# Kernel optimization log

Hardware: AMD Instinct MI355X
Metric: run time of the kernel (lower is better)

Reference implementation:

```python
import jax, jax.numpy as jnp
import numpy as np

N_HOST, N_FLOW, E = 20000, 200000, 600000
D_IN, D_H, D_OUT = 64, 128, 32
NEG_SLOPE = 0.01  # F.leaky_relu default


def setup_inputs() -> dict:
    key = jax.random.key(0)
    ks = jax.random.split(key, 20)

    def w(k, shape):
        # kaiming-uniform-ish init scale (matches Linear fan-in scaling)
        lim = 1.0 / np.sqrt(shape[0])
        return jax.random.uniform(k, shape, jnp.float32, -lim, lim)

    return {
        "x_host": jax.random.normal(ks[0], (N_HOST, D_IN), jnp.float32),
        "x_flow": jax.random.normal(ks[1], (N_FLOW, D_IN), jnp.float32),
        "src_hf": jax.random.randint(ks[2], (E,), 0, N_HOST, dtype=jnp.int32),
        "dst_hf": jax.random.randint(ks[3], (E,), 0, N_FLOW, dtype=jnp.int32),
        "src_fh": jax.random.randint(ks[4], (E,), 0, N_FLOW, dtype=jnp.int32),
        "dst_fh": jax.random.randint(ks[5], (E,), 0, N_HOST, dtype=jnp.int32),
        "W0_hf_l": w(ks[6], (D_IN, D_H)), "W0_hf_r": w(ks[7], (D_IN, D_H)),
        "b0_hf": jnp.zeros((D_H,), jnp.float32),
        "W0_fh_l": w(ks[8], (D_IN, D_H)), "W0_fh_r": w(ks[9], (D_IN, D_H)),
        "b0_fh": jnp.zeros((D_H,), jnp.float32),
        "W1_hf_l": w(ks[10], (D_H, D_H)), "W1_hf_r": w(ks[11], (D_H, D_H)),
        "b1_hf": jnp.zeros((D_H,), jnp.float32),
        "W1_fh_l": w(ks[12], (D_H, D_H)), "W1_fh_r": w(ks[13], (D_H, D_H)),
        "b1_fh": jnp.zeros((D_H,), jnp.float32),
        "W_out": w(ks[14], (D_H, D_OUT)),
        "b_out": jnp.zeros((D_OUT,), jnp.float32),
    }


def _seg_mean(x, src, dst, n_dst):
    """Mean-aggregate src-node features over edges into n_dst segments."""
    s = jax.ops.segment_sum(x[src], dst, num_segments=n_dst)      # [n_dst, d]
    cnt = jax.ops.segment_sum(jnp.ones(src.shape, x.dtype), dst, num_segments=n_dst)
    return s / jnp.clip(cnt, 1.0)[:, None]


def _sage(x_src, x_dst, src, dst, Wl, Wr, b, n_dst):
    # SAGEConv: lin_l(mean_agg) + bias + lin_r(x_dst)
    agg = _seg_mean(x_src, src, dst, n_dst)
    return agg @ Wl + b + x_dst @ Wr


def reference(x_host, x_flow, src_hf, dst_hf, src_fh, dst_fh,
              W0_hf_l, W0_hf_r, b0_hf, W0_fh_l, W0_fh_r, b0_fh,
              W1_hf_l, W1_hf_r, b1_hf, W1_fh_l, W1_fh_r, b1_fh,
              W_out, b_out):
    lrelu = lambda v: jnp.where(v > 0, v, NEG_SLOPE * v)

    # layer 0
    h_flow = lrelu(_sage(x_host, x_flow, src_hf, dst_hf, W0_hf_l, W0_hf_r, b0_hf, N_FLOW))
    h_host = lrelu(_sage(x_flow, x_host, src_fh, dst_fh, W0_fh_l, W0_fh_r, b0_fh, N_HOST))

    # layer 1
    g_flow = lrelu(_sage(h_host, h_flow, src_hf, dst_hf, W1_hf_l, W1_hf_r, b1_hf, N_FLOW))
    g_host = lrelu(_sage(h_flow, h_host, src_fh, dst_fh, W1_fh_l, W1_fh_r, b1_fh, N_HOST))
    del g_host  # computed (matches module) but only 'flow' feeds the head

    return g_flow @ W_out + b_out  # [N_FLOW, D_OUT]
```

## Files before the change

### kernel.cpp

```cpp
#include <hip/hip_runtime.h>


#define N_HOST 20000
#define N_FLOW 200000
#define NEDGE  600000
#define D_IN   64
#define D_H    128
#define D_OUT  32
#define NSEG   (N_FLOW + N_HOST)
#define NBKT_F 196
#define NBKT_H 79
#define NBKT   (NBKT_F + NBKT_H)
#define NEB    586

typedef unsigned short u16;
typedef unsigned int   u32;
typedef short bf16x8 __attribute__((ext_vector_type(8)));
typedef float f32x4  __attribute__((ext_vector_type(4)));

__device__ __forceinline__ float bfh(u16 h) { return __uint_as_float(((u32)h) << 16); }
__device__ __forceinline__ u16 fbh(float f) {
    u32 u = __float_as_uint(f);
    return (u16)((u + 0x7fffu + ((u >> 16) & 1u)) >> 16);
}
__device__ __forceinline__ u32 packbf(float x, float y) {
    return (u32)fbh(x) | ((u32)fbh(y) << 16);
}
__device__ __forceinline__ void acc8(float* a, uint4 u) {
    a[0] += __uint_as_float(u.x << 16);
    a[1] += __uint_as_float(u.x & 0xffff0000u);
    a[2] += __uint_as_float(u.y << 16);
    a[3] += __uint_as_float(u.y & 0xffff0000u);
    a[4] += __uint_as_float(u.z << 16);
    a[5] += __uint_as_float(u.z & 0xffff0000u);
    a[6] += __uint_as_float(u.w << 16);
    a[7] += __uint_as_float(u.w & 0xffff0000u);
}

template <int U>
__device__ __forceinline__ uint4 gmean(const u16* __restrict__ pool, int rs, int coff,
                                       const int* __restrict__ gcsr,
                                       const int* __restrict__ lcsr, int st0, bool fit,
                                       int st, int en) {
    float a[8] = {0.f, 0.f, 0.f, 0.f, 0.f, 0.f, 0.f, 0.f};
    for (int e = st; e < en; e += U) {
        int n[U];
#pragma unroll
        for (int j = 0; j < U; j++)
            n[j] = (e + j < en) ? (fit ? lcsr[e + j - st0] : gcsr[e + j]) : -1;
        uint4 u[U];
#pragma unroll
        for (int j = 0; j < U; j++)
            u[j] = (n[j] >= 0) ? *(const uint4*)(pool + n[j] * rs + coff)
                               : make_uint4(0u, 0u, 0u, 0u);
#pragma unroll
        for (int j = 0; j < U; j++) acc8(a, u[j]);
    }
    float inv = (en > st) ? 1.f / (float)(en - st) : 0.f;
    uint4 o;
    o.x = packbf(a[0] * inv, a[1] * inv);
    o.y = packbf(a[2] * inv, a[3] * inv);
    o.z = packbf(a[4] * inv, a[5] * inv);
    o.w = packbf(a[6] * inv, a[7] * inv);
    return o;
}

__global__ void k_pre(const float* __restrict__ W0_hf_l, const float* __restrict__ W0_hf_r,
                      const float* __restrict__ W0_fh_l, const float* __restrict__ W0_fh_r,
                      const float* __restrict__ W1_l, const float* __restrict__ W1_r,
                      const float* __restrict__ Wout,
                      u16* __restrict__ WT0_hf, u16* __restrict__ WT0_fh,
                      u16* __restrict__ WT1_l, u16* __restrict__ WT1_r,
                      u16* __restrict__ WTo,
                      const float* __restrict__ xf, const float* __restrict__ xh,
                      u16* __restrict__ xfb, u16* __restrict__ xhb,
                      const int* __restrict__ dst_hf, const int* __restrict__ dst_fh,
                      int* __restrict__ bcnt) {
    int b = blockIdx.x, t = threadIdx.x;
    if (b < 34) {
        u16 tmp[8];
        if (b < 32) {
            int e = (b & 7) * 2048 + t * 8;
            int n = e >> 7, k0 = e & 127;
            if (b < 8) {
#pragma unroll
                for (int j = 0; j < 8; j++) {
                    int k = k0 + j;
                    tmp[j] = fbh(k < 64 ? W0_hf_l[k * D_H + n] : W0_hf_r[(k - 64) * D_H + n]);
                }
                *(uint4*)(WT0_hf + n * 128 + k0) = *(uint4*)tmp;
            } else if (b < 16) {
#pragma unroll
                for (int j = 0; j < 8; j++) {
                    int k = k0 + j;
                    tmp[j] = fbh(k < 64 ? W0_fh_l[k * D_H + n] : W0_fh_r[(k - 64) * D_H + n]);
                }
                *(uint4*)(WT0_fh + n * 128 + k0) = *(uint4*)tmp;
            } else if (b < 24) {
#pragma unroll
                for (int j = 0; j < 8; j++) tmp[j] = fbh(W1_l[(k0 + j) * D_H + n]);
                *(uint4*)(WT1_l + n * 128 + k0) = *(uint4*)tmp;
            } else {
#pragma unroll
                for (int j = 0; j < 8; j++) tmp[j] = fbh(W1_r[(k0 + j) * D_H + n]);
                *(uint4*)(WT1_r + n * 128 + k0) = *(uint4*)tmp;
            }
        } else {
            int e = (b - 32) * 2048 + t * 8;
            int n = e >> 7, k0 = e & 127;
#pragma unroll
            for (int j = 0; j < 8; j++) tmp[j] = fbh(Wout[(k0 + j) * D_OUT + n]);
            *(uint4*)(WTo + n * 128 + k0) = *(uint4*)tmp;
        }
    } else if (b < 34 + 6875) {
        int q = (b - 34) * 256 + t;
        const int TF = (N_FLOW * D_IN) / 8;
        const int TT = TF + (N_HOST * D_IN) / 8;
        if (q >= TT) return;
        const float* src; u16* dst; int base;
        if (q < TF) { src = xf; dst = xfb; base = q * 8; }
        else        { src = xh; dst = xhb; base = (q - TF) * 8; }
        float4 f0 = *(const float4*)(src + base);
        float4 f1 = *(const float4*)(src + base + 4);
        uint4 o;
        o.x = packbf(f0.x, f0.y); o.y = packbf(f0.z, f0.w);
        o.z = packbf(f1.x, f1.y); o.w = packbf(f1.z, f1.w);
        *(uint4*)(dst + base) = o;
    } else {
        __shared__ int h[NBKT];
        for (int j = t; j < NBKT; j += 256) h[j] = 0;
        __syncthreads();
        int base = (b - 34 - 6875) * 2048;
#pragma unroll
        for (int i = 0; i < 8; i++) {
            int e = base + t + i * 256;
            if (e < 2 * NEDGE) {
                int bkt = (e < NEDGE) ? (dst_hf[e] >> 10)
                                      : (NBKT_F + (dst_fh[e - NEDGE] >> 8));
                atomicAdd(&h[bkt], 1);
            }
        }
        __syncthreads();
        for (int j = t; j < NBKT; j += 256)
            if (h[j]) atomicAdd(&bcnt[j], h[j]);
    }
}

__global__ void kb2(const int* __restrict__ src_hf, const int* __restrict__ dst_hf,
                    const int* __restrict__ src_fh, const int* __restrict__ dst_fh,
                    const int* __restrict__ bcnt, int* __restrict__ bcur,
                    int2* __restrict__ binE) {
    __shared__ int sp[512];
    __shared__ int lh[NBKT];
    __shared__ int lb[NBKT];
    int t = threadIdx.x;
    int o1 = (t < NBKT) ? bcnt[t] : 0;
    int o2 = (t + 256 < NBKT) ? bcnt[t + 256] : 0;
    sp[t] = o1; sp[t + 256] = o2;
    for (int j = t; j < NBKT; j += 256) lh[j] = 0;
    __syncthreads();
    for (int d = 1; d < 512; d <<= 1) {
        int a0 = (t >= d) ? sp[t - d] : 0;
        int a1 = sp[t + 256 - d];
        __syncthreads();
        sp[t] += a0; sp[t + 256] += a1;
        __syncthreads();
    }
    sp[t] -= o1; sp[t + 256] -= o2;
    __syncthreads();
    int base = blockIdx.x * 2048;
    int mybkt[8], myrank[8], mysrc[8], mydst[8];
#pragma unroll
    for (int i = 0; i < 8; i++) {
        int e = base + t + i * 256;
        mybkt[i] = -1;
        if (e < 2 * NEDGE) {
            int s, d;
            if (e < NEDGE) { s = src_hf[e]; d = dst_hf[e]; }
            else           { s = src_fh[e - NEDGE]; d = dst_fh[e - NEDGE] + N_FLOW; }
            int bkt = (d < N_FLOW) ? (d >> 10) : (NBKT_F + ((d - N_FLOW) >> 8));
            mybkt[i] = bkt; mysrc[i] = s; mydst[i] = d;
            myrank[i] = atomicAdd(&lh[bkt], 1);
        }
    }
    __syncthreads();
    for (int j = t; j < NBKT; j += 256)
        lb[j] = lh[j] ? atomicAdd(&bcur[j], lh[j]) : 0;
    __syncthreads();
#pragma unroll
    for (int i = 0; i < 8; i++) {
        if (mybkt[i] >= 0) {
            int pos = sp[mybkt[i]] + lb[mybkt[i]] + myrank[i];
            binE[pos] = make_int2(mysrc[i], mydst[i]);
        }
    }
}

__global__ __launch_bounds__(256) void kb3(const int2* __restrict__ binE,
                                           const int* __restrict__ bcnt,
                                           int* __restrict__ off, int* __restrict__ csr) {
    __shared__ int sp[512];
    __shared__ int deg[1024];
    __shared__ int ts[256];
    int b = blockIdx.x, t = threadIdx.x;
    sp[t] = (t < NBKT) ? bcnt[t] : 0;
    sp[t + 256] = (t + 256 < NBKT) ? bcnt[t + 256] : 0;
    __syncthreads();
    for (int d = 1; d < 512; d <<= 1) {
        int a0 = (t >= d) ? sp[t - d] : 0;
        int a1 = sp[t + 256 - d];
        __syncthreads();
        sp[t] += a0; sp[t + 256] += a1;
        __syncthreads();
    }
    int e0 = (b == 0) ? 0 : sp[b - 1];
    int e1 = sp[b];
    int nbase, ncnt;
    if (b < NBKT_F) { nbase = b << 10; ncnt = min(1024, N_FLOW - nbase); }
    else { nbase = N_FLOW + ((b - NBKT_F) << 8); ncnt = min(256, NSEG - nbase); }
    for (int i = t; i < 1024; i += 256) deg[i] = 0;
    __syncthreads();
    for (int e = e0 + t; e < e1; e += 256) {
        int2 p = binE[e];
        atomicAdd(&deg[p.y - nbase], 1);
    }
    __syncthreads();
    int loc[4]; int s = 0;
#pragma unroll
    for (int j = 0; j < 4; j++) { loc[j] = s; s += deg[t * 4 + j]; }
    ts[t] = s;
    __syncthreads();
    for (int d = 1; d < 256; d <<= 1) {
        int x = (t >= d) ? ts[t - d] : 0;
        __syncthreads();
        ts[t] += x;
        __syncthreads();
    }
    int base2 = e0 + ts[t] - s;
    int dsave[4];
#pragma unroll
    for (int j = 0; j < 4; j++) dsave[j] = deg[t * 4 + j];
    __syncthreads();
#pragma unroll
    for (int j = 0; j < 4; j++) {
        int idx = t * 4 + j;
        int st = base2 + loc[j];
        deg[idx] = st;
        if (idx < ncnt) off[nbase + idx] = st + dsave[j];
    }
    __syncthreads();
    for (int e = e0 + t; e < e1; e += 256) {
        int2 p = binE[e];
        int r = atomicAdd(&deg[p.y - nbase], 1);
        csr[r] = p.x;
    }
}

__global__ __launch_bounds__(512, 4) void k_host(
    const u16* __restrict__ xfb, const u16* __restrict__ xhb,
    const int* __restrict__ off, const int* __restrict__ csr,
    const u16* __restrict__ WT0, const float* __restrict__ b0,
    const u16* __restrict__ WT1l, u16* __restrict__ hT, int M) {
    __shared__ __align__(16) u16 sA[64 * 136];
    __shared__ int sOff[72];
    __shared__ int sCsr[2560];
    const int t = threadIdx.x;
    const int m0 = blockIdx.x * 64;
    if (t < 65) {
        int idx = N_FLOW + m0 - 1 + t;
        sOff[t] = off[min(idx, NSEG - 1)];
    }
    {
        int r = t >> 3, c = t & 7;
        int row = m0 + r;
        uint4 v = make_uint4(0u, 0u, 0u, 0u);
        if (row < M) v = *(const uint4*)(xhb + row * 64 + c * 8);
        *(uint4*)(&sA[r * 136 + 64 + c * 8]) = v;
    }
    __syncthreads();
    int st0 = sOff[0];
    int win = sOff[64] - st0;
    bool fit = (win <= 2560);
    if (fit) for (int e = t; e < win; e += 512) sCsr[e] = csr[st0 + e];
    __syncthreads();
    {
        int r = t >> 3, c = t & 7;
        int row = m0 + r;
        uint4 o = make_uint4(0u, 0u, 0u, 0u);
        if (row < M) o = gmean<8>(xfb, 64, c * 8, csr, sCsr, st0, fit, sOff[r], sOff[r + 1]);
        *(uint4*)(&sA[r * 136 + c * 8]) = o;
    }
    __syncthreads();
    const int w = t >> 6, wr = w >> 1, wc = w & 1;
    const int ln = t & 63, l15 = ln & 15, quad = ln >> 4;
    const u16* pA = sA + (wr * 16 + l15) * 136 + quad * 8;
    const u16* pB0 = WT0 + wc * 8192 + l15 * 128 + quad * 8;
    f32x4 acc[4];
#pragma unroll
    for (int tt = 0; tt < 4; tt++) acc[tt] = (f32x4){0.f, 0.f, 0.f, 0.f};
#pragma unroll
    for (int s = 0; s < 4; s++) {
        bf16x8 a = *(const bf16x8*)(pA + s * 32);
#pragma unroll
        for (int tt = 0; tt < 4; tt++) {
            bf16x8 b = *(const bf16x8*)(pB0 + tt * 2048 + s * 32);
            acc[tt] = __builtin_amdgcn_mfma_f32_16x16x32_bf16(a, b, acc[tt], 0, 0, 0);
        }
    }
    __syncthreads();
#pragma unroll
    for (int tt = 0; tt < 4; tt++) {
        int col = wc * 64 + tt * 16 + l15;
        float bv = b0[col];
#pragma unroll
        for (int i = 0; i < 4; i++) {
            int rl = wr * 16 + quad * 4 + i;
            float v = acc[tt][i] + bv;
            v = v > 0.f ? v : 0.01f * v;
            sA[rl * 136 + col] = fbh(v);
        }
    }
    __syncthreads();
    const u16* pB1 = WT1l + wc * 8192 + l15 * 128 + quad * 8;
    f32x4 accB[4];
#pragma unroll
    for (int tt = 0; tt < 4; tt++) accB[tt] = (f32x4){0.f, 0.f, 0.f, 0.f};
#pragma unroll
    for (int s = 0; s < 4; s++) {
        bf16x8 a = *(const bf16x8*)(pA + s * 32);
#pragma unroll
        for (int tt = 0; tt < 4; tt++) {
            bf16x8 b = *(const bf16x8*)(pB1 + tt * 2048 + s * 32);
            accB[tt] = __builtin_amdgcn_mfma_f32_16x16x32_bf16(a, b, accB[tt], 0, 0, 0);
        }
    }
#pragma unroll
    for (int tt = 0; tt < 4; tt++) {
        int col = wc * 64 + tt * 16 + l15;
#pragma unroll
        for (int i = 0; i < 4; i++) {
            int row = m0 + wr * 16 + quad * 4 + i;
            if (row < M) hT[row * D_H + col] = fbh(accB[tt][i]);
        }
    }
}

__global__ __launch_bounds__(512, 8) void k_mega(
    const u16* __restrict__ xfb, const u16* __restrict__ xhb,
    const int* __restrict__ off, const int* __restrict__ csr,
    const u16* __restrict__ hT,
    const u16* __restrict__ WT0, const float* __restrict__ b0,
    const u16* __restrict__ WT1r, const float* __restrict__ b1,
    const u16* __restrict__ WTo, const float* __restrict__ bout,
    float* __restrict__ OUT) {
    __shared__ __align__(16) u16 sA[64 * 136];
    __shared__ __align__(16) u16 sAg[64 * 136];
    __shared__ int sOff[72];
    __shared__ int sCsr[1024];
    const int t = threadIdx.x;
    const int m0 = blockIdx.x * 64;
    if (t < 65) {
        int idx = m0 - 1 + t;
        sOff[t] = (idx < 0) ? 0 : off[idx];
    }
    {
        int r = t >> 3, c = t & 7;
        uint4 v = *(const uint4*)(xfb + (m0 + r) * 64 + c * 8);
        *(uint4*)(&sA[r * 136 + 64 + c * 8]) = v;
    }
    __syncthreads();
    int st0 = sOff[0];
    int win = sOff[64] - st0;
    bool fit = (win <= 1024);
    if (fit) for (int e = t; e < win; e += 512) sCsr[e] = csr[st0 + e];
    __syncthreads();
    {
        int r = t >> 3, c = t & 7;
        uint4 o = gmean<4>(xhb, 64, c * 8, csr, sCsr, st0, fit, sOff[r], sOff[r + 1]);
        *(uint4*)(&sA[r * 136 + c * 8]) = o;
    }
#pragma unroll
    for (int i = 0; i < 2; i++) {
        int q = t + i * 512;
        int r = q >> 4, c = q & 15;
        uint4 o = gmean<4>(hT, 128, c * 8, csr, sCsr, st0, fit, sOff[r], sOff[r + 1]);
        *(uint4*)(&sAg[r * 136 + c * 8]) = o;
    }
    __syncthreads();
    const int w = t >> 6, wr = w >> 1, wc = w & 1;
    const int ln = t & 63, l15 = ln & 15, quad = ln >> 4;
    const u16* pA = sA + (wr * 16 + l15) * 136 + quad * 8;
    const u16* pB0 = WT0 + wc * 8192 + l15 * 128 + quad * 8;
    f32x4 acc[4];
#pragma unroll
    for (int tt = 0; tt < 4; tt++) acc[tt] = (f32x4){0.f, 0.f, 0.f, 0.f};
#pragma unroll
    for (int s = 0; s < 4; s++) {
        bf16x8 a = *(const bf16x8*)(pA + s * 32);
#pragma unroll
        for (int tt = 0; tt < 4; tt++) {
            bf16x8 b = *(const bf16x8*)(pB0 + tt * 2048 + s * 32);
            acc[tt] = __builtin_amdgcn_mfma_f32_16x16x32_bf16(a, b, acc[tt], 0, 0, 0);
        }
    }
    __syncthreads();
#pragma unroll
    for (int tt = 0; tt < 4; tt++) {
        int col = wc * 64 + tt * 16 + l15;
        float bv = b0[col];
#pragma unroll
        for (int i = 0; i < 4; i++) {
            int rl = wr * 16 + quad * 4 + i;
            float v = acc[tt][i] + bv;
            v = v > 0.f ? v : 0.01f * v;
            sA[rl * 136 + col] = fbh(v);
        }
    }
    __syncthreads();
    const u16* pB1 = WT1r + wc * 8192 + l15 * 128 + quad * 8;
    f32x4 accB[4];
#pragma unroll
    for (int tt = 0; tt < 4; tt++) accB[tt] = (f32x4){0.f, 0.f, 0.f, 0.f};
#pragma unroll
    for (int s = 0; s < 4; s++) {
        bf16x8 a = *(const bf16x8*)(pA + s * 32);
#pragma unroll
        for (int tt = 0; tt < 4; tt++) {
            bf16x8 b = *(const bf16x8*)(pB1 + tt * 2048 + s * 32);
            accB[tt] = __builtin_amdgcn_mfma_f32_16x16x32_bf16(a, b, accB[tt], 0, 0, 0);
        }
    }
#pragma unroll
    for (int tt = 0; tt < 4; tt++) {
        int col = wc * 64 + tt * 16 + l15;
        float bv = b1[col];
#pragma unroll
        for (int i = 0; i < 4; i++) {
            int rl = wr * 16 + quad * 4 + i;
            float v = accB[tt][i] + bfh(sAg[rl * 136 + col]) + bv;
            v = v > 0.f ? v : 0.01f * v;
            sAg[rl * 136 + col] = fbh(v);
        }
    }
    __syncthreads();
    const u16* pG = sAg + (wr * 16 + l15) * 136 + quad * 8;
    const u16* pBo = WTo + wc * 2048 + l15 * 128 + quad * 8;
    f32x4 acc2 = (f32x4){0.f, 0.f, 0.f, 0.f};
#pragma unroll
    for (int s = 0; s < 4; s++) {
        bf16x8 g = *(const bf16x8*)(pG + s * 32);
        bf16x8 b = *(const bf16x8*)(pBo + s * 32);
        acc2 = __builtin_amdgcn_mfma_f32_16x16x32_bf16(g, b, acc2, 0, 0, 0);
    }
    {
        int col = wc * 16 + l15;
        float bv = bout[col];
#pragma unroll
        for (int i = 0; i < 4; i++) {
            int row = m0 + wr * 16 + quad * 4 + i;
            OUT[row * D_OUT + col] = acc2[i] + bv;
        }
    }
}

extern "C" void kernel_launch(void* const* d_in, const int* in_sizes, int n_in,
                              void* d_out, int out_size, void* d_ws, size_t ws_size,
                              hipStream_t stream) {
    const float* x_host  = (const float*)d_in[0];
    const float* x_flow  = (const float*)d_in[1];
    const int* src_hf  = (const int*)d_in[2];
    const int* dst_hf  = (const int*)d_in[3];
    const int* src_fh  = (const int*)d_in[4];
    const int* dst_fh  = (const int*)d_in[5];
    const float* W0_hf_l = (const float*)d_in[6];
    const float* W0_hf_r = (const float*)d_in[7];
    const float* b0_hf   = (const float*)d_in[8];
    const float* W0_fh_l = (const float*)d_in[9];
    const float* W0_fh_r = (const float*)d_in[10];
    const float* b0_fh   = (const float*)d_in[11];
    const float* W1_hf_l = (const float*)d_in[12];
    const float* W1_hf_r = (const float*)d_in[13];
    const float* b1_hf   = (const float*)d_in[14];
    const float* W_out   = (const float*)d_in[18];
    const float* b_out   = (const float*)d_in[19];
    float* out = (float*)d_out;

    char* ws = (char*)d_ws;
    int*  off    = (int*)(ws + 0);
    int*  csr    = (int*)(ws + 880000);
    u16*  hT     = (u16*)(ws + 5680000);
    u16*  xfb    = (u16*)(ws + 10800000);
    u16*  xhb    = (u16*)(ws + 36400000);
    int2* binE   = (int2*)(ws + 38960000);
    int*  bcnt   = (int*)(ws + 48560000);
    int*  bcur   = (int*)(ws + 48561280);
    u16*  WT0_hf = (u16*)(ws + 48562560);
    u16*  WT0_fh = (u16*)(ws + 48595328);
    u16*  WT1_l  = (u16*)(ws + 48628096);
    u16*  WT1_r  = (u16*)(ws + 48660864);
    u16*  WTo    = (u16*)(ws + 48693632);

    hipMemsetAsync(bcnt, 0, 2560, stream);
    k_pre<<<34 + 6875 + NEB, 256, 0, stream>>>(
        W0_hf_l, W0_hf_r, W0_fh_l, W0_fh_r, W1_hf_l, W1_hf_r, W_out,
        WT0_hf, WT0_fh, WT1_l, WT1_r, WTo,
        x_flow, x_host, xfb, xhb, dst_hf, dst_fh, bcnt);
    kb2<<<NEB, 256, 0, stream>>>(src_hf, dst_hf, src_fh, dst_fh, bcnt, bcur, binE);
    kb3<<<NBKT, 256, 0, stream>>>(binE, bcnt, off, csr);
    k_host<<<313, 512, 0, stream>>>(xfb, xhb, off, csr, WT0_fh, b0_fh, WT1_l, hT, N_HOST);
    k_mega<<<3125, 512, 0, stream>>>(xfb, xhb, off, csr, hT, WT0_hf, b0_hf,
                                     WT1_r, b1_hf, WTo, b_out, out);
}
```

Measured before the change: 344.2 us.

## Split host gather across threads, shrink host tile, fuse flow neighbor gathers

The host kernel now handles 32 rows per block over 625 blocks. Each row's neighbor list is split across two thread halves, and their partial sums are reduced through shared memory, which gives more parallelism on the high-degree host rows (about 30 edges each). The flow mega-kernel fuses its two neighbor gathers (xhb and hT) into one loop that shares the index loads, and accumulation uses packed float2 adds. k_mega launch bounds drop from 8 to 6 waves per SIMD, allowing more registers for the wider gather at the cost of occupancy.

```diff
diff --git a/kernel.cpp b/kernel.cpp
--- a/kernel.cpp
+++ b/kernel.cpp
@@ -17,6 +17,7 @@
 typedef unsigned int   u32;
 typedef short bf16x8 __attribute__((ext_vector_type(8)));
 typedef float f32x4  __attribute__((ext_vector_type(4)));
+typedef float fx2    __attribute__((ext_vector_type(2)));
 
 __device__ __forceinline__ float bfh(u16 h) { return __uint_as_float(((u32)h) << 16); }
 __device__ __forceinline__ u16 fbh(float f) {
@@ -26,42 +27,19 @@
 __device__ __forceinline__ u32 packbf(float x, float y) {
     return (u32)fbh(x) | ((u32)fbh(y) << 16);
 }
-__device__ __forceinline__ void acc8(float* a, uint4 u) {
-    a[0] += __uint_as_float(u.x << 16);
-    a[1] += __uint_as_float(u.x & 0xffff0000u);
-    a[2] += __uint_as_float(u.y << 16);
-    a[3] += __uint_as_float(u.y & 0xffff0000u);
-    a[4] += __uint_as_float(u.z << 16);
-    a[5] += __uint_as_float(u.z & 0xffff0000u);
-    a[6] += __uint_as_float(u.w << 16);
-    a[7] += __uint_as_float(u.w & 0xffff0000u);
-}
-
-template <int U>
-__device__ __forceinline__ uint4 gmean(const u16* __restrict__ pool, int rs, int coff,
-                                       const int* __restrict__ gcsr,
-                                       const int* __restrict__ lcsr, int st0, bool fit,
-                                       int st, int en) {
-    float a[8] = {0.f, 0.f, 0.f, 0.f, 0.f, 0.f, 0.f, 0.f};
-    for (int e = st; e < en; e += U) {
-        int n[U];
-#pragma unroll
-        for (int j = 0; j < U; j++)
-            n[j] = (e + j < en) ? (fit ? lcsr[e + j - st0] : gcsr[e + j]) : -1;
-        uint4 u[U];
-#pragma unroll
-        for (int j = 0; j < U; j++)
-            u[j] = (n[j] >= 0) ? *(const uint4*)(pool + n[j] * rs + coff)
-                               : make_uint4(0u, 0u, 0u, 0u);
-#pragma unroll
-        for (int j = 0; j < U; j++) acc8(a, u[j]);
-    }
-    float inv = (en > st) ? 1.f / (float)(en - st) : 0.f;
+__device__ __forceinline__ void accp(fx2* a, uint4 u) {
+    fx2 p;
+    p.x = __uint_as_float(u.x << 16); p.y = __uint_as_float(u.x & 0xffff0000u); a[0] += p;
+    p.x = __uint_as_float(u.y << 16); p.y = __uint_as_float(u.y & 0xffff0000u); a[1] += p;
+    p.x = __uint_as_float(u.z << 16); p.y = __uint_as_float(u.z & 0xffff0000u); a[2] += p;
+    p.x = __uint_as_float(u.w << 16); p.y = __uint_as_float(u.w & 0xffff0000u); a[3] += p;
+}
+__device__ __forceinline__ uint4 packp(const fx2* a, float inv) {
     uint4 o;
-    o.x = packbf(a[0] * inv, a[1] * inv);
-    o.y = packbf(a[2] * inv, a[3] * inv);
-    o.z = packbf(a[4] * inv, a[5] * inv);
-    o.w = packbf(a[6] * inv, a[7] * inv);
+    o.x = packbf(a[0].x * inv, a[0].y * inv);
+    o.y = packbf(a[1].x * inv, a[1].y * inv);
+    o.z = packbf(a[2].x * inv, a[2].y * inv);
+    o.w = packbf(a[3].x * inv, a[3].y * inv);
     return o;
 }
 
@@ -260,57 +238,78 @@
     const u16* __restrict__ xfb, const u16* __restrict__ xhb,
     const int* __restrict__ off, const int* __restrict__ csr,
     const u16* __restrict__ WT0, const float* __restrict__ b0,
-    const u16* __restrict__ WT1l, u16* __restrict__ hT, int M) {
-    __shared__ __align__(16) u16 sA[64 * 136];
-    __shared__ int sOff[72];
-    __shared__ int sCsr[2560];
+    const u16* __restrict__ WT1l, u16* __restrict__ hT) {
+    __shared__ __align__(16) u16 sA[32 * 136];
+    __shared__ __align__(16) float sP[256 * 8];
+    __shared__ int sOff[40];
+    __shared__ int sCsr[2048];
     const int t = threadIdx.x;
-    const int m0 = blockIdx.x * 64;
-    if (t < 65) {
-        int idx = N_FLOW + m0 - 1 + t;
-        sOff[t] = off[min(idx, NSEG - 1)];
-    }
-    {
+    const int m0 = blockIdx.x * 32;
+    if (t < 33) sOff[t] = off[N_FLOW + m0 - 1 + t];
+    if (t < 256) {
         int r = t >> 3, c = t & 7;
-        int row = m0 + r;
-        uint4 v = make_uint4(0u, 0u, 0u, 0u);
-        if (row < M) v = *(const uint4*)(xhb + row * 64 + c * 8);
+        uint4 v = *(const uint4*)(xhb + (m0 + r) * 64 + c * 8);
         *(uint4*)(&sA[r * 136 + 64 + c * 8]) = v;
     }
     __syncthreads();
     int st0 = sOff[0];
-    int win = sOff[64] - st0;
-    bool fit = (win <= 2560);
+    int win = sOff[32] - st0;
+    bool fit = (win <= 2048);
     if (fit) for (int e = t; e < win; e += 512) sCsr[e] = csr[st0 + e];
     __syncthreads();
-    {
-        int r = t >> 3, c = t & 7;
-        int row = m0 + r;
-        uint4 o = make_uint4(0u, 0u, 0u, 0u);
-        if (row < M) o = gmean<8>(xfb, 64, c * 8, csr, sCsr, st0, fit, sOff[r], sOff[r + 1]);
-        *(uint4*)(&sA[r * 136 + c * 8]) = o;
-    }
-    __syncthreads();
-    const int w = t >> 6, wr = w >> 1, wc = w & 1;
+    const int r = t >> 4, s8 = (t >> 3) & 1, c = t & 7;
+    const int st = sOff[r], en = sOff[r + 1];
+    fx2 a[4] = {};
+    for (int e = st + s8; e < en; e += 16) {
+        int n[8];
+#pragma unroll
+        for (int j = 0; j < 8; j++) {
+            int ee = e + 2 * j;
+            n[j] = (ee < en) ? (fit ? sCsr[ee - st0] : csr[ee]) : -1;
+        }
+        uint4 u[8];
+#pragma unroll
+        for (int j = 0; j < 8; j++)
+            u[j] = (n[j] >= 0) ? *(const uint4*)(xfb + n[j] * 64 + c * 8)
+                               : make_uint4(0u, 0u, 0u, 0u);
+#pragma unroll
+        for (int j = 0; j < 8; j++) accp(a, u[j]);
+    }
+    if (s8) {
+        float4* p = (float4*)(&sP[(r * 8 + c) * 8]);
+        p[0] = make_float4(a[0].x, a[0].y, a[1].x, a[1].y);
+        p[1] = make_float4(a[2].x, a[2].y, a[3].x, a[3].y);
+    }
+    __syncthreads();
+    if (!s8) {
+        const float4* p = (const float4*)(&sP[(r * 8 + c) * 8]);
+        float4 v0 = p[0], v1 = p[1];
+        a[0].x += v0.x; a[0].y += v0.y; a[1].x += v0.z; a[1].y += v0.w;
+        a[2].x += v1.x; a[2].y += v1.y; a[3].x += v1.z; a[3].y += v1.w;
+        float inv = (en > st) ? 1.f / (float)(en - st) : 0.f;
+        *(uint4*)(&sA[r * 136 + c * 8]) = packp(a, inv);
+    }
+    __syncthreads();
+    const int w = t >> 6, wr = w >> 2, wc = w & 3;
     const int ln = t & 63, l15 = ln & 15, quad = ln >> 4;
     const u16* pA = sA + (wr * 16 + l15) * 136 + quad * 8;
-    const u16* pB0 = WT0 + wc * 8192 + l15 * 128 + quad * 8;
-    f32x4 acc[4];
-#pragma unroll
-    for (int tt = 0; tt < 4; tt++) acc[tt] = (f32x4){0.f, 0.f, 0.f, 0.f};
+    const u16* pB0 = WT0 + wc * 4096 + l15 * 128 + quad * 8;
+    f32x4 acc[2];
+    acc[0] = (f32x4){0.f, 0.f, 0.f, 0.f};
+    acc[1] = (f32x4){0.f, 0.f, 0.f, 0.f};
 #pragma unroll
     for (int s = 0; s < 4; s++) {
-        bf16x8 a = *(const bf16x8*)(pA + s * 32);
-#pragma unroll
-        for (int tt = 0; tt < 4; tt++) {
+        bf16x8 av = *(const bf16x8*)(pA + s * 32);
+#pragma unroll
+        for (int tt = 0; tt < 2; tt++) {
             bf16x8 b = *(const bf16x8*)(pB0 + tt * 2048 + s * 32);
-            acc[tt] = __builtin_amdgcn_mfma_f32_16x16x32_bf16(a, b, acc[tt], 0, 0, 0);
-        }
-    }
-    __syncthreads();
-#pragma unroll
-    for (int tt = 0; tt < 4; tt++) {
-        int col = wc * 64 + tt * 16 + l15;
+            acc[tt] = __builtin_amdgcn_mfma_f32_16x16x32_bf16(av, b, acc[tt], 0, 0, 0);
+        }
+    }
+    __syncthreads();
+#pragma unroll
+    for (int tt = 0; tt < 2; tt++) {
+        int col = wc * 32 + tt * 16 + l15;
         float bv = b0[col];
 #pragma unroll
         for (int i = 0; i < 4; i++) {
@@ -321,31 +320,31 @@
         }
     }
     __syncthreads();
-    const u16* pB1 = WT1l + wc * 8192 + l15 * 128 + quad * 8;
-    f32x4 accB[4];
-#pragma unroll
-    for (int tt = 0; tt < 4; tt++) accB[tt] = (f32x4){0.f, 0.f, 0.f, 0.f};
+    const u16* pB1 = WT1l + wc * 4096 + l15 * 128 + quad * 8;
+    f32x4 accB[2];
+    accB[0] = (f32x4){0.f, 0.f, 0.f, 0.f};
+    accB[1] = (f32x4){0.f, 0.f, 0.f, 0.f};
 #pragma unroll
     for (int s = 0; s < 4; s++) {
-        bf16x8 a = *(const bf16x8*)(pA + s * 32);
-#pragma unroll
-        for (int tt = 0; tt < 4; tt++) {
+        bf16x8 av = *(const bf16x8*)(pA + s * 32);
+#pragma unroll
+        for (int tt = 0; tt < 2; tt++) {
             bf16x8 b = *(const bf16x8*)(pB1 + tt * 2048 + s * 32);
-            accB[tt] = __builtin_amdgcn_mfma_f32_16x16x32_bf16(a, b, accB[tt], 0, 0, 0);
-        }
-    }
-#pragma unroll
-    for (int tt = 0; tt < 4; tt++) {
-        int col = wc * 64 + tt * 16 + l15;
+            accB[tt] = __builtin_amdgcn_mfma_f32_16x16x32_bf16(av, b, accB[tt], 0, 0, 0);
+        }
+    }
+#pragma unroll
+    for (int tt = 0; tt < 2; tt++) {
+        int col = wc * 32 + tt * 16 + l15;
 #pragma unroll
         for (int i = 0; i < 4; i++) {
             int row = m0 + wr * 16 + quad * 4 + i;
-            if (row < M) hT[row * D_H + col] = fbh(accB[tt][i]);
-        }
-    }
-}
-
-__global__ __launch_bounds__(512, 8) void k_mega(
+            hT[row * D_H + col] = fbh(accB[tt][i]);
+        }
+    }
+}
+
+__global__ __launch_bounds__(512, 6) void k_mega(
     const u16* __restrict__ xfb, const u16* __restrict__ xhb,
     const int* __restrict__ off, const int* __restrict__ csr,
     const u16* __restrict__ hT,
@@ -375,16 +374,38 @@
     if (fit) for (int e = t; e < win; e += 512) sCsr[e] = csr[st0 + e];
     __syncthreads();
     {
-        int r = t >> 3, c = t & 7;
-        uint4 o = gmean<4>(xhb, 64, c * 8, csr, sCsr, st0, fit, sOff[r], sOff[r + 1]);
-        *(uint4*)(&sA[r * 136 + c * 8]) = o;
-    }
-#pragma unroll
-    for (int i = 0; i < 2; i++) {
-        int q = t + i * 512;
-        int r = q >> 4, c = q & 15;
-        uint4 o = gmean<4>(hT, 128, c * 8, csr, sCsr, st0, fit, sOff[r], sOff[r + 1]);
-        *(uint4*)(&sAg[r * 136 + c * 8]) = o;
+        const int r = t >> 3, c = t & 7;
+        const int st = sOff[r], en = sOff[r + 1];
+        fx2 a0[4] = {}, a1[4] = {}, a2[4] = {};
+        for (int e = st; e < en; e += 4) {
+            int n[4];
+#pragma unroll
+            for (int j = 0; j < 4; j++)
+                n[j] = (e + j < en) ? (fit ? sCsr[e + j - st0] : csr[e + j]) : -1;
+            uint4 ux[4], ua[4], ub[4];
+#pragma unroll
+            for (int j = 0; j < 4; j++) {
+                if (n[j] >= 0) {
+                    const u16* px = xhb + n[j] * 64 + c * 8;
+                    const u16* ph = hT + n[j] * 128 + c * 16;
+                    ux[j] = *(const uint4*)px;
+                    ua[j] = *(const uint4*)ph;
+                    ub[j] = *(const uint4*)(ph + 8);
+                } else {
+                    ux[j] = make_uint4(0u, 0u, 0u, 0u);
+                    ua[j] = make_uint4(0u, 0u, 0u, 0u);
+                    ub[j] = make_uint4(0u, 0u, 0u, 0u);
+                }
+            }
+#pragma unroll
+            for (int j = 0; j < 4; j++) {
+                accp(a0, ux[j]); accp(a1, ua[j]); accp(a2, ub[j]);
+            }
+        }
+        float inv = (en > st) ? 1.f / (float)(en - st) : 0.f;
+        *(uint4*)(&sA[r * 136 + c * 8]) = packp(a0, inv);
+        *(uint4*)(&sAg[r * 136 + c * 16]) = packp(a1, inv);
+        *(uint4*)(&sAg[r * 136 + c * 16 + 8]) = packp(a2, inv);
     }
     __syncthreads();
     const int w = t >> 6, wr = w >> 1, wc = w & 1;
@@ -396,11 +417,11 @@
     for (int tt = 0; tt < 4; tt++) acc[tt] = (f32x4){0.f, 0.f, 0.f, 0.f};
 #pragma unroll
     for (int s = 0; s < 4; s++) {
-        bf16x8 a = *(const bf16x8*)(pA + s * 32);
+        bf16x8 av = *(const bf16x8*)(pA + s * 32);
 #pragma unroll
         for (int tt = 0; tt < 4; tt++) {
             bf16x8 b = *(const bf16x8*)(pB0 + tt * 2048 + s * 32);
-            acc[tt] = __builtin_amdgcn_mfma_f32_16x16x32_bf16(a, b, acc[tt], 0, 0, 0);
+            acc[tt] = __builtin_amdgcn_mfma_f32_16x16x32_bf16(av, b, acc[tt], 0, 0, 0);
         }
     }
     __syncthreads();
@@ -423,11 +444,11 @@
     for (int tt = 0; tt < 4; tt++) accB[tt] = (f32x4){0.f, 0.f, 0.f, 0.f};
 #pragma unroll
     for (int s = 0; s < 4; s++) {
-        bf16x8 a = *(const bf16x8*)(pA + s * 32);
+        bf16x8 av = *(const bf16x8*)(pA + s * 32);
 #pragma unroll
         for (int tt = 0; tt < 4; tt++) {
             bf16x8 b = *(const bf16x8*)(pB1 + tt * 2048 + s * 32);
-            accB[tt] = __builtin_amdgcn_mfma_f32_16x16x32_bf16(a, b, accB[tt], 0, 0, 0);
+            accB[tt] = __builtin_amdgcn_mfma_f32_16x16x32_bf16(av, b, accB[tt], 0, 0, 0);
         }
     }
 #pragma unroll
@@ -507,7 +528,7 @@
         x_flow, x_host, xfb, xhb, dst_hf, dst_fh, bcnt);
     kb2<<<NEB, 256, 0, stream>>>(src_hf, dst_hf, src_fh, dst_fh, bcnt, bcur, binE);
     kb3<<<NBKT, 256, 0, stream>>>(binE, bcnt, off, csr);
-    k_host<<<313, 512, 0, stream>>>(xfb, xhb, off, csr, WT0_fh, b0_fh, WT1_l, hT, N_HOST);
+    k_host<<<625, 512, 0, stream>>>(xfb, xhb, off, csr, WT0_fh, b0_fh, WT1_l, hT);
     k_mega<<<3125, 512, 0, stream>>>(xfb, xhb, off, csr, hT, WT0_hf, b0_hf,
                                      WT1_r, b1_hf, WTo, b_out, out);
 }
```

Measured after the change: 374.4 us. 8.8% more time.
